# Optimization experiments

Hardware: AMD Instinct MI355X
Metric: run time of the kernel (lower is better)

## Reference

```python
import jax, jax.numpy as jnp
import numpy as np
from jax import lax

N_HEAD, D_IN, D_HID, D_OUT = 8, 64, 64, 64
SEQ = 32768
STD = 1.0 / np.sqrt(D_HID * N_HEAD)


def _unif(key, shape):
    return jax.random.uniform(key, shape, jnp.float32, -STD, STD)


def setup_inputs() -> dict:
    key = jax.random.key(0)
    ks = jax.random.split(key, 12)
    D = N_HEAD * D_IN
    return {
        "inputs": jax.random.normal(ks[0], (SEQ, D), jnp.float32),
        "W_in": _unif(ks[1], (D, D)),
        "b_in": _unif(ks[2], (D,)),
        "W_gates": _unif(ks[3], (D_IN, 3 * D_HID)),
        "b_gates": _unif(ks[4], (3 * D_HID,)),
        "W_og": _unif(ks[5], (D_IN, D_HID)),
        "b_og": _unif(ks[6], (D_HID,)),
        "W_c": _unif(ks[7], (D_HID, D_OUT)),
        "b_c": _unif(ks[8], (D_OUT,)),
        "W_out": _unif(ks[9], (N_HEAD * D_OUT, N_HEAD * D_OUT)),
        "b_out": _unif(ks[10], (N_HEAD * D_OUT,)),
    }


def reference(inputs, W_in, b_in, W_gates, b_gates, W_og, b_og, W_c, b_c, W_out, b_out):
    S = inputs.shape[0]
    # input mixing across heads, then flatten: (S, H*d_in) -> (S*H, d_in)
    x = (inputs @ W_in + b_in).reshape(S * N_HEAD, D_IN)
    # FirstModule: fused gate projection
    g = x @ W_gates + b_gates  # (S*H, 3*d_hid)
    fg = jax.nn.sigmoid(g[:, :D_HID])
    ig = jax.nn.sigmoid(g[:, D_HID:2 * D_HID])
    h = jnp.tanh(g[:, 2 * D_HID:])
    hr = ig * h
    # linear recurrence c_t = fg_t * c_{t-1} + hr_t, c_0 = 0, via associative scan
    def comb(e1, e2):
        a1, b1 = e1
        a2, b2 = e2
        return (a1 * a2, b1 * a2 + b2)
    _, c = lax.associative_scan(comb, (fg, hr))  # (S*H, d_hid)
    # SecondModule: output gate and projection
    og = jax.nn.sigmoid(x @ W_og + b_og)
    o = (og * c) @ W_c + b_c  # (S*H, d_out)
    o = o.reshape(S, N_HEAD * D_OUT)
    return o @ W_out + b_out
```

## Files before the change

### kernel.cpp

```cpp
#include <hip/hip_runtime.h>


typedef unsigned short ushort;
typedef __bf16 bf16x8 __attribute__((ext_vector_type(8)));
typedef float f32x4 __attribute__((ext_vector_type(4)));

#define CROWS 64
#define NCH  4096
#define NSUP 64

#define GLOAD16(gp, lp) __builtin_amdgcn_global_load_lds( \
    (const __attribute__((address_space(1))) void*)(gp),  \
    (__attribute__((address_space(3))) void*)(lp), 16, 0, 0)

__device__ inline float b2f(ushort u) {
    return __builtin_bit_cast(float, (unsigned)u << 16);
}
__device__ inline ushort f2b(float f) {
    unsigned x = __builtin_bit_cast(unsigned, f);
    x += 0x7FFFu + ((x >> 16) & 1u);
    return (ushort)(x >> 16);
}
__device__ inline float sigm(float v) { return __builtin_amdgcn_rcpf(1.0f + __expf(-v)); }
__device__ inline float tanh_fast(float v) {
    return 2.0f * __builtin_amdgcn_rcpf(1.0f + __expf(-2.0f * v)) - 1.0f;
}
__device__ inline f32x4 MFMA(bf16x8 a, bf16x8 b, f32x4 c) {
    return __builtin_amdgcn_mfma_f32_16x16x32_bf16(a, b, c, 0, 0, 0);
}

__global__ void transpose512(const float* __restrict__ src, ushort* __restrict__ dst) {
    __shared__ float tile[32][33];
    const int tx = threadIdx.x & 31, ty = threadIdx.x >> 5;
    const int x0 = blockIdx.x * 32, y0 = blockIdx.y * 32;
    #pragma unroll
    for (int dy = 0; dy < 32; dy += 8)
        tile[ty + dy][tx] = src[(size_t)(y0 + ty + dy) * 512 + x0 + tx];
    __syncthreads();
    #pragma unroll
    for (int dy = 0; dy < 32; dy += 8)
        dst[(size_t)(x0 + ty + dy) * 512 + y0 + tx] = f2b(tile[tx][ty + dy]);
}

__global__ void prep_small(const float* __restrict__ W_gates, const float* __restrict__ W_og,
                           const float* __restrict__ W_c,
                           const float* __restrict__ b_gates, const float* __restrict__ b_og,
                           ushort* __restrict__ W2T, ushort* __restrict__ WcT, float* __restrict__ b2) {
    const int idx = blockIdx.x * 256 + threadIdx.x;
    if (idx < 16384) {
        const int n = idx >> 6, k = idx & 63;
        float v;
        if      (n < 64)  v = W_gates[k * 192 + 64 + n];
        else if (n < 128) v = W_gates[k * 192 + 128 + (n - 64)];
        else if (n < 192) v = W_gates[k * 192 + (n - 128)];
        else              v = W_og[k * 64 + (n - 192)];
        W2T[idx] = f2b(v);
    } else if (idx < 16384 + 4096) {
        const int i = idx - 16384;
        const int n = i >> 6, k = i & 63;
        WcT[i] = f2b(W_c[(k << 6) + n]);
    } else if (idx < 16384 + 4096 + 256) {
        const int i = idx - 20480;
        float v;
        if      (i < 64)  v = b_gates[64 + i];
        else if (i < 128) v = b_gates[128 + (i - 64)];
        else if (i < 192) v = b_gates[i - 128];
        else              v = b_og[i - 192];
        b2[i] = v;
    }
}

__global__ __launch_bounds__(256)
void cvt_f32_bf16(const float* __restrict__ src, ushort* __restrict__ dst) {
    const long i = ((long)blockIdx.x * 256 + threadIdx.x) * 8;
    const float4 v0 = *(const float4*)(src + i);
    const float4 v1 = *(const float4*)(src + i + 4);
    *(ushort4*)(dst + i)     = make_ushort4(f2b(v0.x), f2b(v0.y), f2b(v0.z), f2b(v0.w));
    *(ushort4*)(dst + i + 4) = make_ushort4(f2b(v1.x), f2b(v1.y), f2b(v1.z), f2b(v1.w));
}

template <int BM, int BN, int WAVES_M, int WAVES_N, int A32, int C32>
__global__ __launch_bounds__(256)
void gemm_bt(const void* __restrict__ Av, const ushort* __restrict__ Bt,
             const float* __restrict__ bias, void* __restrict__ Cv,
             int M, int N, int K) {
    constexpr int WM = BM / WAVES_M, WN = BN / WAVES_N;
    constexpr int MT = WM / 16, NT = WN / 16;
    __shared__ __align__(16) ushort sA[BM * 32];
    __shared__ __align__(16) ushort sB[BN * 32];

    const int t = threadIdx.x, w = t >> 6, lane = t & 63;
    const int wm = (w / WAVES_N) * WM, wn = (w % WAVES_N) * WN;
    const long bm = (long)blockIdx.x * BM, bn = (long)blockIdx.y * BN;

    f32x4 acc[MT][NT] = {};

    for (int k0 = 0; k0 < K; k0 += 32) {
        if (A32) {
            const float* A = (const float*)Av;
            #pragma unroll
            for (int is = 0; is < BM / 32; ++is) {
                const int row = is * 32 + (t >> 3);
                const int cd = (t & 7) >> 1, half = t & 1;
                const float4 v = *(const float4*)(A + (bm + row) * (long)K + k0 + (t & 7) * 4);
                *(ushort4*)&sA[row * 32 + ((cd ^ (row & 3)) * 8) + half * 4] =
                    make_ushort4(f2b(v.x), f2b(v.y), f2b(v.z), f2b(v.w));
            }
        } else {
            const ushort* A = (const ushort*)Av;
            #pragma unroll
            for (int is = 0; is < BM / 64; ++is) {
                const int row = t >> 2, kc = t & 3;
                GLOAD16(A + (bm + is * 64 + row) * (long)K + k0 + ((kc ^ (row & 3)) * 8),
                        (char*)sA + is * 4096 + w * 1024);
            }
        }
        #pragma unroll
        for (int is = 0; is < BN / 64; ++is) {
            const int row = t >> 2, kc = t & 3;
            GLOAD16(Bt + (bn + is * 64 + row) * (long)K + k0 + ((kc ^ (row & 3)) * 8),
                    (char*)sB + is * 4096 + w * 1024);
        }
        __syncthreads();

        bf16x8 af[MT], bfr[NT];
        #pragma unroll
        for (int i = 0; i < MT; ++i) {
            const int row = wm + i * 16 + (lane & 15), c = lane >> 4;
            af[i] = *(const bf16x8*)&sA[row * 32 + ((c ^ (row & 3)) * 8)];
        }
        #pragma unroll
        for (int j = 0; j < NT; ++j) {
            const int rb = wn + j * 16 + (lane & 15), c = lane >> 4;
            bfr[j] = *(const bf16x8*)&sB[rb * 32 + ((c ^ (rb & 3)) * 8)];
        }
        #pragma unroll
        for (int i = 0; i < MT; ++i)
            #pragma unroll
            for (int j = 0; j < NT; ++j)
                acc[i][j] = MFMA(af[i], bfr[j], acc[i][j]);
        __syncthreads();
    }

    #pragma unroll
    for (int i = 0; i < MT; ++i)
        #pragma unroll
        for (int j = 0; j < NT; ++j) {
            const long col = bn + wn + j * 16 + (lane & 15);
            const float bv = bias[col];
            #pragma unroll
            for (int r = 0; r < 4; ++r) {
                const long row = bm + wm + i * 16 + ((lane >> 4) << 2) + r;
                const float v = acc[i][j][r] + bv;
                if (C32) ((float*)Cv)[row * (long)N + col] = v;
                else     ((ushort*)Cv)[row * (long)N + col] = f2b(v);
            }
        }
}

__global__ __launch_bounds__(256, 4)
void gates_store(const ushort* __restrict__ X, const ushort* __restrict__ W2T,
                 const float* __restrict__ b2,
                 unsigned* __restrict__ FGHR,
                 float* __restrict__ Agg, float* __restrict__ Bgg) {
    __shared__ __align__(16) char smem[20480];
    ushort* sFG = (ushort*)smem;
    ushort* sHR = (ushort*)(smem + 9216);
    float*  spa = (float*)(smem + 18432);
    float*  spb = (float*)(smem + 19456);

    const int t = threadIdx.x, w = t >> 6, lane = t & 63;
    const int blk = blockIdx.x;
    const long row0 = (long)blk * CROWS;

    const int wm = (w >> 1) * 32;
    const int grpB = w & 1;
    const int lr = lane & 15, lc = lane >> 4;

    bf16x8 af[2][2];
    #pragma unroll
    for (int kk = 0; kk < 2; ++kk)
        #pragma unroll
        for (int i = 0; i < 2; ++i)
            af[kk][i] = *(const bf16x8*)(X + (row0 + wm + i * 16 + lr) * 64 + kk * 32 + lc * 8);

    f32x4 acc[2][8] = {};
    if (!grpB) {
        #pragma unroll
        for (int kk = 0; kk < 2; ++kk)
            #pragma unroll
            for (int j = 0; j < 8; ++j) {
                const bf16x8 bf = *(const bf16x8*)(W2T + (j * 16 + lr) * 64 + kk * 32 + lc * 8);
                acc[0][j] = MFMA(af[kk][0], bf, acc[0][j]);
                acc[1][j] = MFMA(af[kk][1], bf, acc[1][j]);
            }
    } else {
        #pragma unroll
        for (int kk = 0; kk < 2; ++kk)
            #pragma unroll
            for (int j = 0; j < 4; ++j) {
                const bf16x8 bf = *(const bf16x8*)(W2T + ((128 + j * 16 + lr)) * 64 + kk * 32 + lc * 8);
                acc[0][j] = MFMA(af[kk][0], bf, acc[0][j]);
                acc[1][j] = MFMA(af[kk][1], bf, acc[1][j]);
            }
    }

    if (!grpB) {
        #pragma unroll
        for (int jj = 0; jj < 4; ++jj) {
            const int ch = jj * 16 + lr;
            const float bi = b2[ch], bh = b2[64 + ch];
            #pragma unroll
            for (int i = 0; i < 2; ++i)
                #pragma unroll
                for (int r = 0; r < 4; ++r) {
                    const int row = wm + i * 16 + (lc << 2) + r;
                    const float gi = acc[i][jj][r] + bi;
                    const float gh = acc[i][jj + 4][r] + bh;
                    sHR[row * 72 + ch] = f2b(sigm(gi) * tanh_fast(gh));
                }
        }
    } else {
        #pragma unroll
        for (int jj = 0; jj < 4; ++jj) {
            const int ch = jj * 16 + lr;
            const float bfg = b2[128 + ch];
            #pragma unroll
            for (int i = 0; i < 2; ++i)
                #pragma unroll
                for (int r = 0; r < 4; ++r) {
                    const int row = wm + i * 16 + (lc << 2) + r;
                    sFG[row * 72 + ch] = f2b(sigm(acc[i][jj][r] + bfg));
                }
        }
    }
    __syncthreads();

    {
        const int ch = lane;
        float a = 1.0f, b = 0.0f;
        #pragma unroll
        for (int r = 0; r < 16; ++r) {
            const int row = (w << 4) + r;
            const ushort ufg = sFG[row * 72 + ch];
            const ushort uhr = sHR[row * 72 + ch];
            FGHR[(row0 + row) * 64 + ch] = (unsigned)ufg | ((unsigned)uhr << 16);
            const float fg = b2f(ufg), hr = b2f(uhr);
            a *= fg;
            b = fmaf(b, fg, hr);
        }
        spa[(w << 6) + ch] = a;
        spb[(w << 6) + ch] = b;
    }
    __syncthreads();

    if (t < 64) {
        float a = spa[t], b = spb[t];
        #pragma unroll
        for (int k = 1; k < 4; ++k) {
            const float a2 = spa[(k << 6) + t];
            const float bb = spb[(k << 6) + t];
            a *= a2;
            b = fmaf(b, a2, bb);
        }
        Agg[blk * 64 + t] = a;
        Bgg[blk * 64 + t] = b;
    }
}

__global__ __launch_bounds__(256, 4)
void scan_apply(const unsigned* __restrict__ FGHR, const ushort* __restrict__ X,
                const ushort* __restrict__ W2T, const float* __restrict__ b2,
                const float* __restrict__ Agg, const float* __restrict__ Bgg,
                const float* __restrict__ PreS,
                const ushort* __restrict__ WcT, const float* __restrict__ b_c,
                ushort* __restrict__ O) {
    __shared__ __align__(16) char smem[19456];
    ushort* sP  = (ushort*)smem;
    ushort* sOG = (ushort*)(smem + 8192);
    float*  spa = (float*)(smem + 17408);
    float*  spb = (float*)(smem + 18432);

    const int t = threadIdx.x, w = t >> 6, lane = t & 63;
    const int blk = blockIdx.x;
    const long row0 = (long)blk * CROWS;
    const int ch = lane;
    const int lr = lane & 15, lc = lane >> 4;
    const int wm = (w >> 1) * 32;
    const int wno = (w & 1) * 32;

    bf16x8 af[2][2], wb[2][2];
    #pragma unroll
    for (int kk = 0; kk < 2; ++kk) {
        #pragma unroll
        for (int i = 0; i < 2; ++i)
            af[kk][i] = *(const bf16x8*)(X + (row0 + wm + i * 16 + lr) * 64 + kk * 32 + lc * 8);
        #pragma unroll
        for (int j = 0; j < 2; ++j)
            wb[kk][j] = *(const bf16x8*)(W2T + (192 + wno + j * 16 + lr) * 64 + kk * 32 + lc * 8);
    }

    unsigned fh[16];
    {
        float a = 1.0f, b = 0.0f;
        #pragma unroll
        for (int r = 0; r < 16; ++r) {
            fh[r] = FGHR[(row0 + (w << 4) + r) * 64 + ch];
            const float fg = b2f((ushort)fh[r]);
            const float hr = b2f((ushort)(fh[r] >> 16));
            a *= fg;
            b = fmaf(b, fg, hr);
        }
        spa[(w << 6) + ch] = a;
        spb[(w << 6) + ch] = b;
    }

    {
        f32x4 aog[2][2] = {};
        #pragma unroll
        for (int kk = 0; kk < 2; ++kk)
            #pragma unroll
            for (int i = 0; i < 2; ++i)
                #pragma unroll
                for (int j = 0; j < 2; ++j)
                    aog[i][j] = MFMA(af[kk][i], wb[kk][j], aog[i][j]);
        #pragma unroll
        for (int i = 0; i < 2; ++i)
            #pragma unroll
            for (int j = 0; j < 2; ++j) {
                const int col = wno + j * 16 + lr;
                const float bog = b2[192 + col];
                #pragma unroll
                for (int r = 0; r < 4; ++r) {
                    const int row = wm + i * 16 + (lc << 2) + r;
                    sOG[row * 72 + col] = f2b(sigm(aog[i][j][r] + bog));
                }
            }
    }
    __syncthreads();

    float c = fmaf(PreS[(blk >> 6) * 64 + ch], Agg[blk * 64 + ch], Bgg[blk * 64 + ch]);
    for (int k = 0; k < w; ++k)
        c = fmaf(c, spa[(k << 6) + ch], spb[(k << 6) + ch]);

    const int cch = ch >> 3, half = ch & 7;
    #pragma unroll
    for (int r = 0; r < 16; ++r) {
        const int row = (w << 4) + r;
        const float fg = b2f((ushort)fh[r]);
        const float hr = b2f((ushort)(fh[r] >> 16));
        c = fmaf(c, fg, hr);
        const float og = b2f(sOG[row * 72 + ch]);
        sP[row * 64 + ((cch ^ (row & 7)) * 8) + half] = f2b(og * c);
    }
    __syncthreads();

    f32x4 acc2[2][2] = {};
    #pragma unroll
    for (int kk = 0; kk < 2; ++kk) {
        bf16x8 pa[2], wc[2];
        #pragma unroll
        for (int i = 0; i < 2; ++i) {
            const int row = wm + i * 16 + lr, cidx = kk * 4 + lc;
            pa[i] = *(const bf16x8*)&sP[row * 64 + ((cidx ^ (row & 7)) * 8)];
        }
        #pragma unroll
        for (int j = 0; j < 2; ++j)
            wc[j] = *(const bf16x8*)(WcT + (wno + j * 16 + lr) * 64 + kk * 32 + lc * 8);
        #pragma unroll
        for (int i = 0; i < 2; ++i)
            #pragma unroll
            for (int j = 0; j < 2; ++j)
                acc2[i][j] = MFMA(pa[i], wc[j], acc2[i][j]);
    }
    #pragma unroll
    for (int i = 0; i < 2; ++i)
        #pragma unroll
        for (int j = 0; j < 2; ++j) {
            const int col = wno + j * 16 + lr;
            const float bv = b_c[col];
            #pragma unroll
            for (int r = 0; r < 4; ++r) {
                const int row = wm + i * 16 + (lc << 2) + r;
                O[(row0 + row) * 64 + col] = f2b(acc2[i][j][r] + bv);
            }
        }
}

template <int APPLY>
__global__ __launch_bounds__(256, 4)
void gates_scan(const ushort* __restrict__ X, const ushort* __restrict__ W2T,
                const float* __restrict__ b2, const ushort* __restrict__ WcT,
                const float* __restrict__ b_c,
                float* __restrict__ Agg, float* __restrict__ Bgg,
                const float* __restrict__ PreS, ushort* __restrict__ O) {
    __shared__ __align__(16) char smem[APPLY ? 35840 : 18432];
    ushort* sFG = (ushort*)smem;
    ushort* sHR = (ushort*)(smem + 9216);
    ushort* sOG = (ushort*)(smem + 18432);
    ushort* sP  = (ushort*)(smem + 27648);

    const int t = threadIdx.x, w = t >> 6, lane = t & 63;
    const int blk = blockIdx.x;
    const long row0 = (long)blk * CROWS;

    const int wm = (w >> 1) * 32;
    const int grpB = w & 1;
    const int colbase = grpB * 128;
    const int lr = lane & 15, lc = lane >> 4;

    bf16x8 af[2][2];
    #pragma unroll
    for (int kk = 0; kk < 2; ++kk)
        #pragma unroll
        for (int i = 0; i < 2; ++i)
            af[kk][i] = *(const bf16x8*)(X + (row0 + wm + i * 16 + lr) * 64 + kk * 32 + lc * 8);

    f32x4 acc[2][8] = {};
    #pragma unroll
    for (int kk = 0; kk < 2; ++kk)
        #pragma unroll
        for (int j = 0; j < 8; ++j) {
            const bf16x8 bf = *(const bf16x8*)(W2T + (colbase + j * 16 + lr) * 64 + kk * 32 + lc * 8);
            acc[0][j] = MFMA(af[kk][0], bf, acc[0][j]);
            acc[1][j] = MFMA(af[kk][1], bf, acc[1][j]);
        }

    if (!grpB) {
        #pragma unroll
        for (int jj = 0; jj < 4; ++jj) {
            const int ch = jj * 16 + lr;
            const float bi = b2[ch], bh = b2[64 + ch];
            #pragma unroll
            for (int i = 0; i < 2; ++i)
                #pragma unroll
                for (int r = 0; r < 4; ++r) {
                    const int row = wm + i * 16 + (lc << 2) + r;
                    const float gi = acc[i][jj][r] + bi;
                    const float gh = acc[i][jj + 4][r] + bh;
                    sHR[row * 72 + ch] = f2b(sigm(gi) * tanh_fast(gh));
                }
        }
    } else {
        #pragma unroll
        for (int jj = 0; jj < 4; ++jj) {
            const int ch = jj * 16 + lr;
            const float bfg = b2[128 + ch], bog = b2[192 + ch];
            #pragma unroll
            for (int i = 0; i < 2; ++i)
                #pragma unroll
                for (int r = 0; r < 4; ++r) {
                    const int row = wm + i * 16 + (lc << 2) + r;
                    sFG[row * 72 + ch] = f2b(sigm(acc[i][jj][r] + bfg));
                    if (APPLY) sOG[row * 72 + ch] = f2b(sigm(acc[i][jj + 4][r] + bog));
                }
        }
    }
    __syncthreads();

    if (!APPLY) {
        if (t < 64) {
            float a = 1.0f, b = 0.0f;
            #pragma unroll 8
            for (int r = 0; r < CROWS; ++r) {
                const float fg = b2f(sFG[r * 72 + t]);
                const float hr = b2f(sHR[r * 72 + t]);
                a *= fg;
                b = fmaf(b, fg, hr);
            }
            Agg[blk * 64 + t] = a;
            Bgg[blk * 64 + t] = b;
        }
        return;
    }

    if (t < 64) {
        float c = fmaf(PreS[(blk >> 6) * 64 + t], Agg[blk * 64 + t], Bgg[blk * 64 + t]);
        const int cch = t >> 3, half = t & 7;
        #pragma unroll 8
        for (int r = 0; r < CROWS; ++r) {
            const float fg = b2f(sFG[r * 72 + t]);
            const float hr = b2f(sHR[r * 72 + t]);
            c = fmaf(c, fg, hr);
            sP[r * 64 + ((cch ^ (r & 7)) * 8) + half] = f2b(b2f(sOG[r * 72 + t]) * c);
        }
    }
    __syncthreads();

    const int wn2 = grpB * 32;
    f32x4 acc2[2][2] = {};
    #pragma unroll
    for (int kk = 0; kk < 2; ++kk) {
        bf16x8 pa[2], wbx[2];
        #pragma unroll
        for (int i = 0; i < 2; ++i) {
            const int row = wm + i * 16 + lr, c = kk * 4 + lc;
            pa[i] = *(const bf16x8*)&sP[row * 64 + ((c ^ (row & 7)) * 8)];
        }
        #pragma unroll
        for (int j = 0; j < 2; ++j)
            wbx[j] = *(const bf16x8*)(WcT + (wn2 + j * 16 + lr) * 64 + kk * 32 + lc * 8);
        #pragma unroll
        for (int i = 0; i < 2; ++i)
            #pragma unroll
            for (int j = 0; j < 2; ++j)
                acc2[i][j] = MFMA(pa[i], wbx[j], acc2[i][j]);
    }
    #pragma unroll
    for (int i = 0; i < 2; ++i)
        #pragma unroll
        for (int j = 0; j < 2; ++j) {
            const int col = wn2 + j * 16 + lr;
            const float bv = b_c[col];
            #pragma unroll
            for (int r = 0; r < 4; ++r) {
                const int row = wm + i * 16 + (lc << 2) + r;
                O[(row0 + row) * 64 + col] = f2b(acc2[i][j][r] + bv);
            }
        }
}

__global__ void scan_super(float* __restrict__ Agg, float* __restrict__ Bgg,
                           float* __restrict__ SA, float* __restrict__ SB) {
    const int s = blockIdx.x, ch = threadIdx.x;
    float a = 1.0f, b = 0.0f;
    #pragma unroll 8
    for (int j = 0; j < 64; ++j) {
        const int idx = (s * 64 + j) * 64 + ch;
        const float a2 = Agg[idx], bb = Bgg[idx];
        Agg[idx] = a;
        Bgg[idx] = b;
        a *= a2;
        b = fmaf(b, a2, bb);
    }
    SA[s * 64 + ch] = a;
    SB[s * 64 + ch] = b;
}

__global__ void scan_top(const float* __restrict__ SA, const float* __restrict__ SB,
                         float* __restrict__ PreS) {
    const int ch = threadIdx.x;
    float c = 0.0f;
    #pragma unroll 8
    for (int s = 0; s < 64; ++s) {
        PreS[s * 64 + ch] = c;
        c = fmaf(c, SA[s * 64 + ch], SB[s * 64 + ch]);
    }
}

extern "C" void kernel_launch(void* const* d_in, const int* in_sizes, int n_in,
                              void* d_out, int out_size, void* d_ws, size_t ws_size,
                              hipStream_t stream) {
    const float* inputs  = (const float*)d_in[0];
    const float* W_in    = (const float*)d_in[1];
    const float* b_in    = (const float*)d_in[2];
    const float* W_gates = (const float*)d_in[3];
    const float* b_gates = (const float*)d_in[4];
    const float* W_og    = (const float*)d_in[5];
    const float* b_og    = (const float*)d_in[6];
    const float* W_c     = (const float*)d_in[7];
    const float* b_c     = (const float*)d_in[8];
    const float* W_out   = (const float*)d_in[9];
    const float* b_out   = (const float*)d_in[10];
    float* out = (float*)d_out;

    char* ws = (char*)d_ws;
    ushort* X     = (ushort*)(ws);
    ushort* WinT  = (ushort*)(ws + 33554432);
    ushort* WoutT = (ushort*)(ws + 34078720);
    ushort* W2T   = (ushort*)(ws + 34603008);
    ushort* WcT   = (ushort*)(ws + 34635776);
    float*  b2    = (float*)(ws + 34643968);
    float*  Agg   = (float*)(ws + 34644992);
    float*  Bgg   = (float*)(ws + 35693568);
    float*  SA    = (float*)(ws + 36742144);
    float*  SB    = (float*)(ws + 36758528);
    float*  PreS  = (float*)(ws + 36774912);
    ushort* Ibf   = (ushort*)(ws + 36791296);
    unsigned* FGHR = (unsigned*)(ws + 36791296);
    ushort* O = X;

    const bool new_path = ws_size >= 103900160ull;
    const bool big_ws   = ws_size >= 70345728ull;

    transpose512<<<dim3(16, 16), 256, 0, stream>>>(W_in, WinT);
    transpose512<<<dim3(16, 16), 256, 0, stream>>>(W_out, WoutT);
    prep_small<<<81, 256, 0, stream>>>(W_gates, W_og, W_c, b_gates, b_og, W2T, WcT, b2);

    if (new_path) {
        cvt_f32_bf16<<<8192, 256, 0, stream>>>(inputs, Ibf);
        gemm_bt<128, 128, 2, 2, 0, 0><<<dim3(256, 4), 256, 0, stream>>>(
            Ibf, WinT, b_in, X, 32768, 512, 512);
        gates_store<<<NCH, 256, 0, stream>>>(X, W2T, b2, FGHR, Agg, Bgg);
        scan_super<<<NSUP, 64, 0, stream>>>(Agg, Bgg, SA, SB);
        scan_top<<<1, 64, 0, stream>>>(SA, SB, PreS);
        scan_apply<<<NCH, 256, 0, stream>>>(FGHR, X, W2T, b2, Agg, Bgg, PreS, WcT, b_c, O);
    } else if (big_ws) {
        cvt_f32_bf16<<<8192, 256, 0, stream>>>(inputs, Ibf);
        gemm_bt<128, 128, 2, 2, 0, 0><<<dim3(256, 4), 256, 0, stream>>>(
            Ibf, WinT, b_in, X, 32768, 512, 512);
        gates_scan<0><<<NCH, 256, 0, stream>>>(X, W2T, b2, WcT, b_c, Agg, Bgg, PreS, O);
        scan_super<<<NSUP, 64, 0, stream>>>(Agg, Bgg, SA, SB);
        scan_top<<<1, 64, 0, stream>>>(SA, SB, PreS);
        gates_scan<1><<<NCH, 256, 0, stream>>>(X, W2T, b2, WcT, b_c, Agg, Bgg, PreS, O);
    } else {
        gemm_bt<128, 128, 2, 2, 1, 0><<<dim3(256, 4), 256, 0, stream>>>(
            inputs, WinT, b_in, X, 32768, 512, 512);
        gates_scan<0><<<NCH, 256, 0, stream>>>(X, W2T, b2, WcT, b_c, Agg, Bgg, PreS, O);
        scan_super<<<NSUP, 64, 0, stream>>>(Agg, Bgg, SA, SB);
        scan_top<<<1, 64, 0, stream>>>(SA, SB, PreS);
        gates_scan<1><<<NCH, 256, 0, stream>>>(X, W2T, b2, WcT, b_c, Agg, Bgg, PreS, O);
    }

    gemm_bt<128, 128, 2, 2, 0, 1><<<dim3(256, 4), 256, 0, stream>>>(
        O, WoutT, b_out, out, 32768, 512, 512);
}
```

Before: 289.0 us.

## Give each wave its own 16 rows with all gate columns, dropping a block barrier

Each wave now computes all 192 gate columns for a private 16-row slice, instead of pairs of waves splitting rows 32-wide and splitting the columns into hr and fg groups. Each wave writes packed fg/hr words into its own XOR-swizzled LDS region and then reads them back itself for the local scan, so the block-wide barrier before the scan is removed and the LDS footprint shrinks. The work per wave is now balanced, where before the fg-only waves did less. In exchange, each wave loads the whole weight tile and keeps 12 accumulators live, which adds register and global/L2 load pressure.

```diff
diff --git a/kernel.cpp b/kernel.cpp
--- a/kernel.cpp
+++ b/kernel.cpp
@@ -163,89 +163,53 @@
                  const float* __restrict__ b2,
                  unsigned* __restrict__ FGHR,
                  float* __restrict__ Agg, float* __restrict__ Bgg) {
-    __shared__ __align__(16) char smem[20480];
-    ushort* sFG = (ushort*)smem;
-    ushort* sHR = (ushort*)(smem + 9216);
-    float*  spa = (float*)(smem + 18432);
-    float*  spb = (float*)(smem + 19456);
+    __shared__ __align__(16) char smem[18432];
+    unsigned* sW  = (unsigned*)smem;
+    float*    spa = (float*)(smem + 16384);
+    float*    spb = (float*)(smem + 17408);
 
     const int t = threadIdx.x, w = t >> 6, lane = t & 63;
     const int blk = blockIdx.x;
     const long row0 = (long)blk * CROWS;
-
-    const int wm = (w >> 1) * 32;
-    const int grpB = w & 1;
     const int lr = lane & 15, lc = lane >> 4;
 
-    bf16x8 af[2][2];
+    bf16x8 af[2];
     #pragma unroll
     for (int kk = 0; kk < 2; ++kk)
-        #pragma unroll
-        for (int i = 0; i < 2; ++i)
-            af[kk][i] = *(const bf16x8*)(X + (row0 + wm + i * 16 + lr) * 64 + kk * 32 + lc * 8);
-
-    f32x4 acc[2][8] = {};
-    if (!grpB) {
-        #pragma unroll
-        for (int kk = 0; kk < 2; ++kk)
-            #pragma unroll
-            for (int j = 0; j < 8; ++j) {
-                const bf16x8 bf = *(const bf16x8*)(W2T + (j * 16 + lr) * 64 + kk * 32 + lc * 8);
-                acc[0][j] = MFMA(af[kk][0], bf, acc[0][j]);
-                acc[1][j] = MFMA(af[kk][1], bf, acc[1][j]);
-            }
-    } else {
-        #pragma unroll
-        for (int kk = 0; kk < 2; ++kk)
-            #pragma unroll
-            for (int j = 0; j < 4; ++j) {
-                const bf16x8 bf = *(const bf16x8*)(W2T + ((128 + j * 16 + lr)) * 64 + kk * 32 + lc * 8);
-                acc[0][j] = MFMA(af[kk][0], bf, acc[0][j]);
-                acc[1][j] = MFMA(af[kk][1], bf, acc[1][j]);
-            }
-    }
-
-    if (!grpB) {
-        #pragma unroll
-        for (int jj = 0; jj < 4; ++jj) {
-            const int ch = jj * 16 + lr;
-            const float bi = b2[ch], bh = b2[64 + ch];
-            #pragma unroll
-            for (int i = 0; i < 2; ++i)
-                #pragma unroll
-                for (int r = 0; r < 4; ++r) {
-                    const int row = wm + i * 16 + (lc << 2) + r;
-                    const float gi = acc[i][jj][r] + bi;
-                    const float gh = acc[i][jj + 4][r] + bh;
-                    sHR[row * 72 + ch] = f2b(sigm(gi) * tanh_fast(gh));
-                }
-        }
-    } else {
-        #pragma unroll
-        for (int jj = 0; jj < 4; ++jj) {
-            const int ch = jj * 16 + lr;
-            const float bfg = b2[128 + ch];
-            #pragma unroll
-            for (int i = 0; i < 2; ++i)
-                #pragma unroll
-                for (int r = 0; r < 4; ++r) {
-                    const int row = wm + i * 16 + (lc << 2) + r;
-                    sFG[row * 72 + ch] = f2b(sigm(acc[i][jj][r] + bfg));
-                }
-        }
-    }
-    __syncthreads();
+        af[kk] = *(const bf16x8*)(X + (row0 + (w << 4) + lr) * 64 + kk * 32 + lc * 8);
+
+    f32x4 acc[12] = {};
+    #pragma unroll
+    for (int kk = 0; kk < 2; ++kk)
+        #pragma unroll
+        for (int j = 0; j < 12; ++j) {
+            const bf16x8 bf = *(const bf16x8*)(W2T + (j * 16 + lr) * 64 + kk * 32 + lc * 8);
+            acc[j] = MFMA(af[kk], bf, acc[j]);
+        }
+
+    #pragma unroll
+    for (int jj = 0; jj < 4; ++jj) {
+        const int ch = jj * 16 + lr;
+        const float bi = b2[ch], bh = b2[64 + ch], bfg = b2[128 + ch];
+        #pragma unroll
+        for (int r = 0; r < 4; ++r) {
+            const int row = (lc << 2) + r;
+            const float hr = sigm(acc[jj][r] + bi) * tanh_fast(acc[4 + jj][r] + bh);
+            const float fg = sigm(acc[8 + jj][r] + bfg);
+            sW[(w << 10) + row * 64 + (ch ^ (lc << 4))] =
+                (unsigned)f2b(fg) | ((unsigned)f2b(hr) << 16);
+        }
+    }
 
     {
         const int ch = lane;
         float a = 1.0f, b = 0.0f;
         #pragma unroll
         for (int r = 0; r < 16; ++r) {
-            const int row = (w << 4) + r;
-            const ushort ufg = sFG[row * 72 + ch];
-            const ushort uhr = sHR[row * 72 + ch];
-            FGHR[(row0 + row) * 64 + ch] = (unsigned)ufg | ((unsigned)uhr << 16);
-            const float fg = b2f(ufg), hr = b2f(uhr);
+            const unsigned fh = sW[(w << 10) + r * 64 + (ch ^ ((r >> 2) << 4))];
+            FGHR[(row0 + (w << 4) + r) * 64 + ch] = fh;
+            const float fg = b2f((ushort)fh);
+            const float hr = b2f((ushort)(fh >> 16));
             a *= fg;
             b = fmaf(b, fg, hr);
         }
```

Result: slower. 303.5 us (+5.0%).
